# Optimization experiments

Hardware: AMD Instinct MI355X
Metric: run time of the kernel (lower is better)

Reference implementation:

```python
import jax, jax.numpy as jnp
import numpy as np

PATCH = 16
TOP_K = 5
EPS = 1e-12


def l2_normalize(x, axis):
    sq = jnp.sum(x * x, axis=axis, keepdims=True)
    return x * jax.lax.rsqrt(jnp.maximum(sq, EPS))


def patch_embed(imgs, conv_w, conv_b):
    # imgs: (P, 3, 32, 32) -> (P, n_patches=4, D=768)
    y = jax.lax.conv_general_dilated(
        imgs, conv_w, window_strides=(PATCH, PATCH), padding='VALID',
        dimension_numbers=('NCHW', 'OIHW', 'NCHW'))  # (P, D, 2, 2)
    y = y + conv_b[None, :, None, None]
    P, D = y.shape[0], y.shape[1]
    return y.reshape(P, D, -1).transpose(0, 2, 1)  # (P, 4, D)


def setup_inputs() -> dict:
    key = jax.random.key(0)
    k1, k2, k3, k4 = jax.random.split(key, 4)
    B, N, D = 256, 196, 768
    P = 32  # pool_size
    x_embed = jax.random.normal(k1, (B, N, D), dtype=jnp.float32)
    # uniform(-1, 1) init as in the torch module
    prompt = jax.random.uniform(k2, (P, 3, 32, 32), dtype=jnp.float32, minval=-1.0, maxval=1.0)
    prompt_key = jax.random.uniform(k3, (P, D), dtype=jnp.float32, minval=-1.0, maxval=1.0)
    conv_w = jax.random.normal(k4, (D, 3, PATCH, PATCH), dtype=jnp.float32) * 0.02
    conv_b = jnp.zeros((D,), dtype=jnp.float32)
    return {'x_embed': x_embed, 'prompt': prompt, 'prompt_key': prompt_key,
            'conv_w': conv_w, 'conv_b': conv_b}


def reference(x_embed, prompt, prompt_key, conv_w, conv_b):
    B = x_embed.shape[0]
    prompt_embed = patch_embed(prompt, conv_w, conv_b)      # (P, 4, D)

    x_embed_mean = jnp.mean(x_embed, axis=1)                # (B, D), embedding_key='mean'
    prompt_norm = l2_normalize(prompt_key, axis=1)          # (P, D)
    x_embed_norm = l2_normalize(x_embed_mean, axis=1)       # (B, D)
    similarity = x_embed_norm @ prompt_norm.T               # (B, P)

    _, idx = jax.lax.top_k(similarity, TOP_K)               # (B, top_k)

    batched_prompt_embed = prompt_embed[idx]                # (B, top_k, 4, D)
    Bq, K, L, D = batched_prompt_embed.shape
    batched_prompt_embed = batched_prompt_embed.reshape(Bq, K * L, D)

    batched_key_norm = prompt_norm[idx]                     # (B, top_k, D)
    reduce_sim = jnp.sum(batched_key_norm * x_embed_norm[:, None, :]) / B

    prompted_embedding = jnp.concatenate([batched_prompt_embed, x_embed], axis=1)
    return prompted_embedding, reduce_sim, similarity, idx
```

## Files before the change

kernel.cpp:

```cpp
#include <hip/hip_runtime.h>

typedef unsigned short u16;
typedef unsigned int u32;
typedef float __attribute__((ext_vector_type(4))) f32x4;

#define BB 256
#define NN 196
#define DD 768
#define PP 32
#define TOPK 5
#define NROW 216

#define OUT0_ELTS (BB * NROW * DD)
#define RS_OFF    OUT0_ELTS
#define SIM_OFF   (OUT0_ELTS + 1)
#define IDX_OFF   (OUT0_ELTS + 1 + BB * PP)

#define WS_PNORM  0
#define WS_PEMB   98304
#define WS_IDX    491520

__global__ __launch_bounds__(256) void k_prep(const float* __restrict__ pkey,
                                              const float* __restrict__ prompt,
                                              const float* __restrict__ cw,
                                              const float* __restrict__ cb,
                                              float* __restrict__ pnorm,
                                              float* __restrict__ pemb) {
    const int t = threadIdx.x;
    if (blockIdx.x < PP) {
        const int p = blockIdx.x;
        const float* row = pkey + (size_t)p * DD;
        float v0 = row[t], v1 = row[t + 256], v2 = row[t + 512];
        float sq = v0 * v0 + v1 * v1 + v2 * v2;
#pragma unroll
        for (int off = 32; off; off >>= 1) sq += __shfl_down(sq, off);
        __shared__ float wsum[4];
        __shared__ float rshared;
        if ((t & 63) == 0) wsum[t >> 6] = sq;
        __syncthreads();
        if (t == 0) rshared = rsqrtf(fmaxf(wsum[0] + wsum[1] + wsum[2] + wsum[3], 1e-12f));
        __syncthreads();
        float r = rshared;
        float* orow = pnorm + (size_t)p * DD;
        orow[t] = v0 * r;
        orow[t + 256] = v1 * r;
        orow[t + 512] = v2 * r;
    } else {
        const int bxx = blockIdx.x - PP;
        const int chunk = bxx / 32, pg = bxx - chunk * 32;
        const int m0 = pg * 4;
        const int n = chunk * 256 + t;
        __shared__ float patch[4 * DD];
        for (int idx = t; idx < 4 * DD; idx += 256) {
            const int j = idx / DD, kk = idx - j * DD;
            const int c = kk >> 8, rem = kk & 255;
            const int kh = rem >> 4, kw = rem & 15;
            const int m = m0 + j;
            const int p = m >> 2, l = m & 3;
            patch[idx] = prompt[(size_t)p * 3072 + (size_t)c * 1024
                                + ((l >> 1) * 16 + kh) * 32 + (l & 1) * 16 + kw];
        }
        __syncthreads();
        const float4* wrow = (const float4*)(cw + (size_t)n * DD);
        const float4* p0 = (const float4*)(patch);
        const float4* p1 = (const float4*)(patch + DD);
        const float4* p2 = (const float4*)(patch + 2 * DD);
        const float4* p3 = (const float4*)(patch + 3 * DD);
        float a0 = 0.f, a1 = 0.f, a2 = 0.f, a3 = 0.f;
#pragma unroll 4
        for (int kk = 0; kk < 192; ++kk) {
            const float4 w = wrow[kk];
            const float4 q0 = p0[kk], q1 = p1[kk], q2 = p2[kk], q3 = p3[kk];
            a0 += q0.x * w.x + q0.y * w.y + q0.z * w.z + q0.w * w.w;
            a1 += q1.x * w.x + q1.y * w.y + q1.z * w.z + q1.w * w.w;
            a2 += q2.x * w.x + q2.y * w.y + q2.z * w.z + q2.w * w.w;
            a3 += q3.x * w.x + q3.y * w.y + q3.z * w.z + q3.w * w.w;
        }
        const float bias = cb[n];
        pemb[(size_t)(m0 + 0) * DD + n] = a0 + bias;
        pemb[(size_t)(m0 + 1) * DD + n] = a1 + bias;
        pemb[(size_t)(m0 + 2) * DD + n] = a2 + bias;
        pemb[(size_t)(m0 + 3) * DD + n] = a3 + bias;
    }
}

__global__ __launch_bounds__(768) void k_fused(const float* __restrict__ x,
                                               const float* __restrict__ pnorm,
                                               const float* __restrict__ pemb,
                                               float* __restrict__ out,
                                               int* __restrict__ idx_ws) {
    const int b = blockIdx.x;
    const int t = threadIdx.x;
    const int g = t / 192, c = t - g * 192;
    const float* xb = x + (size_t)b * (NN * DD);
    float* ob = out + (size_t)b * (NROW * DD) + 20 * DD;
    f32x4 s = (f32x4)(0.f);
#pragma unroll
    for (int o = 0; o < 7; ++o) {
        f32x4 vv[7];
#pragma unroll
        for (int i = 0; i < 7; ++i) {
            const int row = g + 4 * (o * 7 + i);
            vv[i] = __builtin_nontemporal_load((const f32x4*)(xb + (size_t)row * DD) + c);
        }
#pragma unroll
        for (int i = 0; i < 7; ++i) {
            const int row = g + 4 * (o * 7 + i);
            s += vv[i];
            __builtin_nontemporal_store(vv[i], (f32x4*)(ob + (size_t)row * DD) + c);
        }
    }
    __shared__ f32x4 comb[768];
    __shared__ float xm[768];
    __shared__ float sims[PP];
    __shared__ float wred[12];
    __shared__ float rsh;
    __shared__ int lidx[TOPK];
    comb[g * 192 + c] = s;
    __syncthreads();
    if (g == 0) {
        f32x4 s0 = comb[c], s1 = comb[192 + c], s2 = comb[384 + c], s3 = comb[576 + c];
        const float inv = 1.0f / NN;
        f32x4 m4 = (s0 + s1 + s2 + s3) * inv;
        xm[4 * c + 0] = m4.x;
        xm[4 * c + 1] = m4.y;
        xm[4 * c + 2] = m4.z;
        xm[4 * c + 3] = m4.w;
    }
    __syncthreads();
    float sq = xm[t] * xm[t];
#pragma unroll
    for (int off = 32; off; off >>= 1) sq += __shfl_down(sq, off);
    if ((t & 63) == 0) wred[t >> 6] = sq;
    __syncthreads();
    if (t == 0) {
        float tot = 0.f;
        for (int i = 0; i < 12; ++i) tot += wred[i];
        rsh = rsqrtf(fmaxf(tot, 1e-12f));
    }
    __syncthreads();
    const float r = rsh;
    if (t < 512) {
        const int p = t >> 4, sub = t & 15;
        const float* pr = pnorm + (size_t)p * DD;
        float acc = 0.f;
#pragma unroll 8
        for (int j = 0; j < 48; ++j) {
            const int k = sub + (j << 4);
            acc += xm[k] * pr[k];
        }
        acc += __shfl_down(acc, 8, 16);
        acc += __shfl_down(acc, 4, 16);
        acc += __shfl_down(acc, 2, 16);
        acc += __shfl_down(acc, 1, 16);
        if (sub == 0) {
            const float sv = acc * r;
            sims[p] = sv;
            out[SIM_OFF + b * PP + p] = sv;
        }
    }
    __syncthreads();
    if (t < 64) {
        float v = (t < PP) ? sims[t] : -1e30f;
#pragma unroll
        for (int k = 0; k < TOPK; ++k) {
            float bv = v; int bbi = t;
#pragma unroll
            for (int off = 32; off; off >>= 1) {
                const float ov = __shfl_xor(bv, off);
                const int   oi = __shfl_xor(bbi, off);
                if (ov > bv || (ov == bv && oi < bbi)) { bv = ov; bbi = oi; }
            }
            if (t == 0) {
                lidx[k] = bbi;
                idx_ws[b * TOPK + k] = bbi;
                out[IDX_OFF + b * TOPK + k] = (float)bbi;
            }
            if (t == bbi) v = -1e30f;
        }
    }
    __syncthreads();
    f32x4* dst = (f32x4*)(out + (size_t)b * (NROW * DD));
    const f32x4* src = (const f32x4*)pemb;
    for (int v = t; v < 20 * 192; v += 768) {
        const int row = v / 192;
        const int off = v - row * 192;
        const int srow = lidx[row >> 2] * 4 + (row & 3);
        __builtin_nontemporal_store(src[srow * 192 + off], dst + row * 192 + off);
    }
}

__global__ __launch_bounds__(256) void k_final(const float* __restrict__ out_sim,
                                               const int* __restrict__ idx_ws,
                                               float* __restrict__ out_rs) {
    const int t = threadIdx.x;
    float s = 0.f;
#pragma unroll
    for (int k = 0; k < TOPK; ++k)
        s += out_sim[t * PP + idx_ws[t * TOPK + k]];
#pragma unroll
    for (int off = 32; off; off >>= 1) s += __shfl_down(s, off);
    __shared__ float wsum[4];
    if ((t & 63) == 0) wsum[t >> 6] = s;
    __syncthreads();
    if (t == 0) *out_rs = (wsum[0] + wsum[1] + wsum[2] + wsum[3]) * (1.0f / BB);
}

extern "C" void kernel_launch(void* const* d_in, const int* in_sizes, int n_in,
                              void* d_out, int out_size, void* d_ws, size_t ws_size,
                              hipStream_t stream) {
    const float* x      = (const float*)d_in[0];
    const float* prompt = (const float*)d_in[1];
    const float* pkey   = (const float*)d_in[2];
    const float* cw     = (const float*)d_in[3];
    const float* cb     = (const float*)d_in[4];
    float* out = (float*)d_out;
    char* ws = (char*)d_ws;

    float* pnorm = (float*)(ws + WS_PNORM);
    float* pemb  = (float*)(ws + WS_PEMB);
    int*   idxw  = (int*)(ws + WS_IDX);

    k_prep<<<PP + 96, 256, 0, stream>>>(pkey, prompt, cw, cb, pnorm, pemb);
    k_fused<<<BB, 768, 0, stream>>>(x, pnorm, pemb, out, idxw);
    k_final<<<1, 256, 0, stream>>>(out + SIM_OFF, idxw, out + RS_OFF);
}
```

Measured before the change: 329.8 us.

## Fuse prep, main and final kernels into one cooperative kernel with grid syncs

The three launches are merged into a single cooperative kernel. The prompt-key normalisation and the patch-embedding conv are spread across the first 64 blocks, and the conv math is interleaved with the streaming copy of x. Grid-wide syncs replace the kernel boundaries, and the reduce_sim sum now uses partials from the top-k values. This removes launch gaps and the serial prep stage, but adds two grid barriers and a cooperative-launch occupancy requirement (256 blocks of 768 threads must be co-resident).

```diff
diff --git a/kernel.cpp b/kernel.cpp
--- a/kernel.cpp
+++ b/kernel.cpp
@@ -1,7 +1,8 @@
 #include <hip/hip_runtime.h>
-
-typedef unsigned short u16;
-typedef unsigned int u32;
+#include <hip/hip_cooperative_groups.h>
+
+namespace cg = cooperative_groups;
+
 typedef float __attribute__((ext_vector_type(4))) f32x4;
 
 #define BB 256
@@ -18,110 +19,108 @@
 
 #define WS_PNORM  0
 #define WS_PEMB   98304
-#define WS_IDX    491520
-
-__global__ __launch_bounds__(256) void k_prep(const float* __restrict__ pkey,
-                                              const float* __restrict__ prompt,
-                                              const float* __restrict__ cw,
-                                              const float* __restrict__ cb,
-                                              float* __restrict__ pnorm,
-                                              float* __restrict__ pemb) {
-    const int t = threadIdx.x;
-    if (blockIdx.x < PP) {
-        const int p = blockIdx.x;
-        const float* row = pkey + (size_t)p * DD;
-        float v0 = row[t], v1 = row[t + 256], v2 = row[t + 512];
-        float sq = v0 * v0 + v1 * v1 + v2 * v2;
-#pragma unroll
-        for (int off = 32; off; off >>= 1) sq += __shfl_down(sq, off);
-        __shared__ float wsum[4];
-        __shared__ float rshared;
-        if ((t & 63) == 0) wsum[t >> 6] = sq;
-        __syncthreads();
-        if (t == 0) rshared = rsqrtf(fmaxf(wsum[0] + wsum[1] + wsum[2] + wsum[3], 1e-12f));
-        __syncthreads();
-        float r = rshared;
-        float* orow = pnorm + (size_t)p * DD;
-        orow[t] = v0 * r;
-        orow[t + 256] = v1 * r;
-        orow[t + 512] = v2 * r;
-    } else {
-        const int bxx = blockIdx.x - PP;
-        const int chunk = bxx / 32, pg = bxx - chunk * 32;
-        const int m0 = pg * 4;
-        const int n = chunk * 256 + t;
-        __shared__ float patch[4 * DD];
-        for (int idx = t; idx < 4 * DD; idx += 256) {
-            const int j = idx / DD, kk = idx - j * DD;
-            const int c = kk >> 8, rem = kk & 255;
-            const int kh = rem >> 4, kw = rem & 15;
-            const int m = m0 + j;
-            const int p = m >> 2, l = m & 3;
-            patch[idx] = prompt[(size_t)p * 3072 + (size_t)c * 1024
-                                + ((l >> 1) * 16 + kh) * 32 + (l & 1) * 16 + kw];
-        }
-        __syncthreads();
-        const float4* wrow = (const float4*)(cw + (size_t)n * DD);
-        const float4* p0 = (const float4*)(patch);
-        const float4* p1 = (const float4*)(patch + DD);
-        const float4* p2 = (const float4*)(patch + 2 * DD);
-        const float4* p3 = (const float4*)(patch + 3 * DD);
-        float a0 = 0.f, a1 = 0.f, a2 = 0.f, a3 = 0.f;
-#pragma unroll 4
-        for (int kk = 0; kk < 192; ++kk) {
-            const float4 w = wrow[kk];
-            const float4 q0 = p0[kk], q1 = p1[kk], q2 = p2[kk], q3 = p3[kk];
-            a0 += q0.x * w.x + q0.y * w.y + q0.z * w.z + q0.w * w.w;
-            a1 += q1.x * w.x + q1.y * w.y + q1.z * w.z + q1.w * w.w;
-            a2 += q2.x * w.x + q2.y * w.y + q2.z * w.z + q2.w * w.w;
-            a3 += q3.x * w.x + q3.y * w.y + q3.z * w.z + q3.w * w.w;
-        }
-        const float bias = cb[n];
-        pemb[(size_t)(m0 + 0) * DD + n] = a0 + bias;
-        pemb[(size_t)(m0 + 1) * DD + n] = a1 + bias;
-        pemb[(size_t)(m0 + 2) * DD + n] = a2 + bias;
-        pemb[(size_t)(m0 + 3) * DD + n] = a3 + bias;
-    }
-}
-
-__global__ __launch_bounds__(768) void k_fused(const float* __restrict__ x,
-                                               const float* __restrict__ pnorm,
-                                               const float* __restrict__ pemb,
-                                               float* __restrict__ out,
-                                               int* __restrict__ idx_ws) {
+#define WS_PART   491520
+
+__global__ __launch_bounds__(768, 3) void k_all(
+    const float* __restrict__ x, const float* __restrict__ prompt,
+    const float* __restrict__ pkey, const float* __restrict__ cw,
+    const float* __restrict__ cb, float* __restrict__ out,
+    float* __restrict__ pnorm, float* __restrict__ pemb,
+    float* __restrict__ wspart)
+{
     const int b = blockIdx.x;
     const int t = threadIdx.x;
-    const int g = t / 192, c = t - g * 192;
-    const float* xb = x + (size_t)b * (NN * DD);
-    float* ob = out + (size_t)b * (NROW * DD) + 20 * DD;
-    f32x4 s = (f32x4)(0.f);
-#pragma unroll
-    for (int o = 0; o < 7; ++o) {
-        f32x4 vv[7];
-#pragma unroll
-        for (int i = 0; i < 7; ++i) {
-            const int row = g + 4 * (o * 7 + i);
-            vv[i] = __builtin_nontemporal_load((const f32x4*)(xb + (size_t)row * DD) + c);
-        }
-#pragma unroll
-        for (int i = 0; i < 7; ++i) {
-            const int row = g + 4 * (o * 7 + i);
-            s += vv[i];
-            __builtin_nontemporal_store(vv[i], (f32x4*)(ob + (size_t)row * DD) + c);
-        }
-    }
+
+    __shared__ float patch[4 * DD];
     __shared__ f32x4 comb[768];
     __shared__ float xm[768];
     __shared__ float sims[PP];
     __shared__ float wred[12];
     __shared__ float rsh;
     __shared__ int lidx[TOPK];
+
+    const bool is_pemb = (b < PP);
+
+    if (b >= PP && b < 2 * PP) {
+        const int p = b - PP;
+        const float v = pkey[(size_t)p * DD + t];
+        float sq = v * v;
+#pragma unroll
+        for (int off = 32; off; off >>= 1) sq += __shfl_down(sq, off);
+        if ((t & 63) == 0) wred[t >> 6] = sq;
+        __syncthreads();
+        if (t == 0) {
+            float tot = 0.f;
+            for (int i = 0; i < 12; ++i) tot += wred[i];
+            rsh = rsqrtf(fmaxf(tot, 1e-12f));
+        }
+        __syncthreads();
+        pnorm[(size_t)p * DD + t] = v * rsh;
+    }
+
+    if (is_pemb) {
+        for (int idx = t; idx < 4 * DD; idx += 768) {
+            const int j = idx / DD, kk = idx - j * DD;
+            const int ch = kk >> 8, rem = kk & 255;
+            const int kh = rem >> 4, kw = rem & 15;
+            patch[idx] = prompt[(size_t)b * 3072 + (size_t)ch * 1024
+                                + ((j >> 1) * 16 + kh) * 32 + (j & 1) * 16 + kw];
+        }
+    }
+    __syncthreads();
+
+    const int g = t / 192, c = t - g * 192;
+    const float* xb = x + (size_t)b * (NN * DD);
+    float* ob = out + (size_t)b * (NROW * DD) + 20 * DD;
+    const float4* wrow = (const float4*)(cw + (size_t)t * DD);
+    const float4* q0p = (const float4*)(patch);
+    const float4* q1p = (const float4*)(patch + DD);
+    const float4* q2p = (const float4*)(patch + 2 * DD);
+    const float4* q3p = (const float4*)(patch + 3 * DD);
+    float a0 = 0.f, a1 = 0.f, a2 = 0.f, a3 = 0.f;
+    f32x4 s = (f32x4)(0.f);
+#pragma unroll
+    for (int o = 0; o < 7; ++o) {
+        f32x4 vv[7];
+#pragma unroll
+        for (int i = 0; i < 7; ++i) {
+            const int row = g + 4 * (o * 7 + i);
+            vv[i] = __builtin_nontemporal_load((const f32x4*)(xb + (size_t)row * DD) + c);
+        }
+        if (is_pemb) {
+            const int k0 = o * 28;
+            const int k1 = (o == 6) ? 192 : (k0 + 28);
+#pragma unroll 4
+            for (int kk = k0; kk < k1; ++kk) {
+                const float4 w = wrow[kk];
+                const float4 q0 = q0p[kk], q1 = q1p[kk], q2 = q2p[kk], q3 = q3p[kk];
+                a0 += q0.x * w.x + q0.y * w.y + q0.z * w.z + q0.w * w.w;
+                a1 += q1.x * w.x + q1.y * w.y + q1.z * w.z + q1.w * w.w;
+                a2 += q2.x * w.x + q2.y * w.y + q2.z * w.z + q2.w * w.w;
+                a3 += q3.x * w.x + q3.y * w.y + q3.z * w.z + q3.w * w.w;
+            }
+        }
+#pragma unroll
+        for (int i = 0; i < 7; ++i) {
+            const int row = g + 4 * (o * 7 + i);
+            s += vv[i];
+            __builtin_nontemporal_store(vv[i], (f32x4*)(ob + (size_t)row * DD) + c);
+        }
+    }
+    if (is_pemb) {
+        const float bias = cb[t];
+        float* pe = pemb + (size_t)(4 * b) * DD + t;
+        pe[0]      = a0 + bias;
+        pe[DD]     = a1 + bias;
+        pe[2 * DD] = a2 + bias;
+        pe[3 * DD] = a3 + bias;
+    }
+
     comb[g * 192 + c] = s;
     __syncthreads();
     if (g == 0) {
         f32x4 s0 = comb[c], s1 = comb[192 + c], s2 = comb[384 + c], s3 = comb[576 + c];
-        const float inv = 1.0f / NN;
-        f32x4 m4 = (s0 + s1 + s2 + s3) * inv;
+        f32x4 m4 = (s0 + s1 + s2 + s3) * (1.0f / NN);
         xm[4 * c + 0] = m4.x;
         xm[4 * c + 1] = m4.y;
         xm[4 * c + 2] = m4.z;
@@ -140,6 +139,10 @@
     }
     __syncthreads();
     const float r = rsh;
+
+    __threadfence();
+    cg::this_grid().sync();
+
     if (t < 512) {
         const int p = t >> 4, sub = t & 15;
         const float* pr = pnorm + (size_t)p * DD;
@@ -160,8 +163,10 @@
         }
     }
     __syncthreads();
+
     if (t < 64) {
         float v = (t < PP) ? sims[t] : -1e30f;
+        float rsum = 0.f;
 #pragma unroll
         for (int k = 0; k < TOPK; ++k) {
             float bv = v; int bbi = t;
@@ -173,13 +178,15 @@
             }
             if (t == 0) {
                 lidx[k] = bbi;
-                idx_ws[b * TOPK + k] = bbi;
                 out[IDX_OFF + b * TOPK + k] = (float)bbi;
+                rsum += bv;
             }
             if (t == bbi) v = -1e30f;
         }
-    }
-    __syncthreads();
+        if (t == 0) wspart[b] = rsum;
+    }
+    __syncthreads();
+
     f32x4* dst = (f32x4*)(out + (size_t)b * (NROW * DD));
     const f32x4* src = (const f32x4*)pemb;
     for (int v = t; v < 20 * 192; v += 768) {
@@ -188,22 +195,21 @@
         const int srow = lidx[row >> 2] * 4 + (row & 3);
         __builtin_nontemporal_store(src[srow * 192 + off], dst + row * 192 + off);
     }
-}
-
-__global__ __launch_bounds__(256) void k_final(const float* __restrict__ out_sim,
-                                               const int* __restrict__ idx_ws,
-                                               float* __restrict__ out_rs) {
-    const int t = threadIdx.x;
-    float s = 0.f;
-#pragma unroll
-    for (int k = 0; k < TOPK; ++k)
-        s += out_sim[t * PP + idx_ws[t * TOPK + k]];
-#pragma unroll
-    for (int off = 32; off; off >>= 1) s += __shfl_down(s, off);
-    __shared__ float wsum[4];
-    if ((t & 63) == 0) wsum[t >> 6] = s;
-    __syncthreads();
-    if (t == 0) *out_rs = (wsum[0] + wsum[1] + wsum[2] + wsum[3]) * (1.0f / BB);
+
+    __threadfence();
+    cg::this_grid().sync();
+    if (b == 0) {
+        float sv = (t < BB) ? wspart[t] : 0.f;
+#pragma unroll
+        for (int off = 32; off; off >>= 1) sv += __shfl_down(sv, off);
+        if ((t & 63) == 0) wred[t >> 6] = sv;
+        __syncthreads();
+        if (t == 0) {
+            float tot = 0.f;
+            for (int i = 0; i < 12; ++i) tot += wred[i];
+            out[RS_OFF] = tot * (1.0f / BB);
+        }
+    }
 }
 
 extern "C" void kernel_launch(void* const* d_in, const int* in_sizes, int n_in,
@@ -217,11 +223,11 @@
     float* out = (float*)d_out;
     char* ws = (char*)d_ws;
 
-    float* pnorm = (float*)(ws + WS_PNORM);
-    float* pemb  = (float*)(ws + WS_PEMB);
-    int*   idxw  = (int*)(ws + WS_IDX);
-
-    k_prep<<<PP + 96, 256, 0, stream>>>(pkey, prompt, cw, cb, pnorm, pemb);
-    k_fused<<<BB, 768, 0, stream>>>(x, pnorm, pemb, out, idxw);
-    k_final<<<1, 256, 0, stream>>>(out + SIM_OFF, idxw, out + RS_OFF);
+    float* pnorm  = (float*)(ws + WS_PNORM);
+    float* pemb   = (float*)(ws + WS_PEMB);
+    float* wspart = (float*)(ws + WS_PART);
+
+    void* args[] = {(void*)&x, (void*)&prompt, (void*)&pkey, (void*)&cw, (void*)&cb,
+                    (void*)&out, (void*)&pnorm, (void*)&pemb, (void*)&wspart};
+    hipLaunchCooperativeKernel((void*)k_all, dim3(BB), dim3(768), args, 0, stream);
 }
```

Result: slower. 615.9 us (+86.8%).

## Fuse key normalization and reduce_sim into main kernel, double-buffer x loads

Applied to the files above, without the earlier changes.

Drops the separate final kernel by having each block atomically add its top-k similarity sum into reduce_sim, after a memset zeroes that slot. Prompt-key normalization moves out of the prep kernel: each block recomputes the key norms alongside the similarity dot products. The x copy loop is software-pipelined so the next 7-row group is loaded while the current one is stored. This removes one launch and a workspace round trip, but adds a memset, redundant norm work in every block, and a float atomic whose summation order is nondeterministic.

```diff
diff --git a/kernel.cpp b/kernel.cpp
--- a/kernel.cpp
+++ b/kernel.cpp
@@ -1,7 +1,5 @@
 #include <hip/hip_runtime.h>
 
-typedef unsigned short u16;
-typedef unsigned int u32;
 typedef float __attribute__((ext_vector_type(4))) f32x4;
 
 #define BB 256
@@ -16,99 +14,81 @@
 #define SIM_OFF   (OUT0_ELTS + 1)
 #define IDX_OFF   (OUT0_ELTS + 1 + BB * PP)
 
-#define WS_PNORM  0
-#define WS_PEMB   98304
-#define WS_IDX    491520
+#define WS_PEMB   0
 
-__global__ __launch_bounds__(256) void k_prep(const float* __restrict__ pkey,
-                                              const float* __restrict__ prompt,
+__global__ __launch_bounds__(256) void k_prep(const float* __restrict__ prompt,
                                               const float* __restrict__ cw,
                                               const float* __restrict__ cb,
-                                              float* __restrict__ pnorm,
                                               float* __restrict__ pemb) {
     const int t = threadIdx.x;
-    if (blockIdx.x < PP) {
-        const int p = blockIdx.x;
-        const float* row = pkey + (size_t)p * DD;
-        float v0 = row[t], v1 = row[t + 256], v2 = row[t + 512];
-        float sq = v0 * v0 + v1 * v1 + v2 * v2;
-#pragma unroll
-        for (int off = 32; off; off >>= 1) sq += __shfl_down(sq, off);
-        __shared__ float wsum[4];
-        __shared__ float rshared;
-        if ((t & 63) == 0) wsum[t >> 6] = sq;
-        __syncthreads();
-        if (t == 0) rshared = rsqrtf(fmaxf(wsum[0] + wsum[1] + wsum[2] + wsum[3], 1e-12f));
-        __syncthreads();
-        float r = rshared;
-        float* orow = pnorm + (size_t)p * DD;
-        orow[t] = v0 * r;
-        orow[t + 256] = v1 * r;
-        orow[t + 512] = v2 * r;
-    } else {
-        const int bxx = blockIdx.x - PP;
-        const int chunk = bxx / 32, pg = bxx - chunk * 32;
-        const int m0 = pg * 4;
-        const int n = chunk * 256 + t;
-        __shared__ float patch[4 * DD];
-        for (int idx = t; idx < 4 * DD; idx += 256) {
-            const int j = idx / DD, kk = idx - j * DD;
-            const int c = kk >> 8, rem = kk & 255;
-            const int kh = rem >> 4, kw = rem & 15;
-            const int m = m0 + j;
-            const int p = m >> 2, l = m & 3;
-            patch[idx] = prompt[(size_t)p * 3072 + (size_t)c * 1024
-                                + ((l >> 1) * 16 + kh) * 32 + (l & 1) * 16 + kw];
-        }
-        __syncthreads();
-        const float4* wrow = (const float4*)(cw + (size_t)n * DD);
-        const float4* p0 = (const float4*)(patch);
-        const float4* p1 = (const float4*)(patch + DD);
-        const float4* p2 = (const float4*)(patch + 2 * DD);
-        const float4* p3 = (const float4*)(patch + 3 * DD);
-        float a0 = 0.f, a1 = 0.f, a2 = 0.f, a3 = 0.f;
+    const int bxx = blockIdx.x;
+    const int chunk = bxx / 32, pg = bxx - chunk * 32;
+    const int m0 = pg * 4;
+    const int n = chunk * 256 + t;
+    __shared__ float patch[4 * DD];
+    for (int idx = t; idx < 4 * DD; idx += 256) {
+        const int j = idx / DD, kk = idx - j * DD;
+        const int c = kk >> 8, rem = kk & 255;
+        const int kh = rem >> 4, kw = rem & 15;
+        const int m = m0 + j;
+        const int p = m >> 2, l = m & 3;
+        patch[idx] = prompt[(size_t)p * 3072 + (size_t)c * 1024
+                            + ((l >> 1) * 16 + kh) * 32 + (l & 1) * 16 + kw];
+    }
+    __syncthreads();
+    const float4* wrow = (const float4*)(cw + (size_t)n * DD);
+    const float4* p0 = (const float4*)(patch);
+    const float4* p1 = (const float4*)(patch + DD);
+    const float4* p2 = (const float4*)(patch + 2 * DD);
+    const float4* p3 = (const float4*)(patch + 3 * DD);
+    float a0 = 0.f, a1 = 0.f, a2 = 0.f, a3 = 0.f;
 #pragma unroll 4
-        for (int kk = 0; kk < 192; ++kk) {
-            const float4 w = wrow[kk];
-            const float4 q0 = p0[kk], q1 = p1[kk], q2 = p2[kk], q3 = p3[kk];
-            a0 += q0.x * w.x + q0.y * w.y + q0.z * w.z + q0.w * w.w;
-            a1 += q1.x * w.x + q1.y * w.y + q1.z * w.z + q1.w * w.w;
-            a2 += q2.x * w.x + q2.y * w.y + q2.z * w.z + q2.w * w.w;
-            a3 += q3.x * w.x + q3.y * w.y + q3.z * w.z + q3.w * w.w;
-        }
-        const float bias = cb[n];
-        pemb[(size_t)(m0 + 0) * DD + n] = a0 + bias;
-        pemb[(size_t)(m0 + 1) * DD + n] = a1 + bias;
-        pemb[(size_t)(m0 + 2) * DD + n] = a2 + bias;
-        pemb[(size_t)(m0 + 3) * DD + n] = a3 + bias;
+    for (int kk = 0; kk < 192; ++kk) {
+        const float4 w = wrow[kk];
+        const float4 q0 = p0[kk], q1 = p1[kk], q2 = p2[kk], q3 = p3[kk];
+        a0 += q0.x * w.x + q0.y * w.y + q0.z * w.z + q0.w * w.w;
+        a1 += q1.x * w.x + q1.y * w.y + q1.z * w.z + q1.w * w.w;
+        a2 += q2.x * w.x + q2.y * w.y + q2.z * w.z + q2.w * w.w;
+        a3 += q3.x * w.x + q3.y * w.y + q3.z * w.z + q3.w * w.w;
     }
+    const float bias = cb[n];
+    pemb[(size_t)(m0 + 0) * DD + n] = a0 + bias;
+    pemb[(size_t)(m0 + 1) * DD + n] = a1 + bias;
+    pemb[(size_t)(m0 + 2) * DD + n] = a2 + bias;
+    pemb[(size_t)(m0 + 3) * DD + n] = a3 + bias;
 }
 
 __global__ __launch_bounds__(768) void k_fused(const float* __restrict__ x,
-                                               const float* __restrict__ pnorm,
+                                               const float* __restrict__ pkey,
                                                const float* __restrict__ pemb,
-                                               float* __restrict__ out,
-                                               int* __restrict__ idx_ws) {
+                                               float* __restrict__ out) {
     const int b = blockIdx.x;
     const int t = threadIdx.x;
     const int g = t / 192, c = t - g * 192;
     const float* xb = x + (size_t)b * (NN * DD);
     float* ob = out + (size_t)b * (NROW * DD) + 20 * DD;
     f32x4 s = (f32x4)(0.f);
+    f32x4 va[7], vb[7];
+#pragma unroll
+    for (int i = 0; i < 7; ++i)
+        va[i] = __builtin_nontemporal_load((const f32x4*)(xb + (size_t)(g + 4 * i) * DD) + c);
 #pragma unroll
     for (int o = 0; o < 7; ++o) {
-        f32x4 vv[7];
+        if (o < 6) {
 #pragma unroll
-        for (int i = 0; i < 7; ++i) {
-            const int row = g + 4 * (o * 7 + i);
-            vv[i] = __builtin_nontemporal_load((const f32x4*)(xb + (size_t)row * DD) + c);
+            for (int i = 0; i < 7; ++i) {
+                const int row = g + 4 * ((o + 1) * 7 + i);
+                vb[i] = __builtin_nontemporal_load((const f32x4*)(xb + (size_t)row * DD) + c);
+            }
         }
 #pragma unroll
         for (int i = 0; i < 7; ++i) {
             const int row = g + 4 * (o * 7 + i);
-            s += vv[i];
-            __builtin_nontemporal_store(vv[i], (f32x4*)(ob + (size_t)row * DD) + c);
+            s += va[i];
+            __builtin_nontemporal_store(va[i], (f32x4*)(ob + (size_t)row * DD) + c);
         }
+#pragma unroll
+        for (int i = 0; i < 7; ++i) va[i] = vb[i];
     }
     __shared__ f32x4 comb[768];
     __shared__ float xm[768];
@@ -120,8 +100,7 @@
     __syncthreads();
     if (g == 0) {
         f32x4 s0 = comb[c], s1 = comb[192 + c], s2 = comb[384 + c], s3 = comb[576 + c];
-        const float inv = 1.0f / NN;
-        f32x4 m4 = (s0 + s1 + s2 + s3) * inv;
+        f32x4 m4 = (s0 + s1 + s2 + s3) * (1.0f / NN);
         xm[4 * c + 0] = m4.x;
         xm[4 * c + 1] = m4.y;
         xm[4 * c + 2] = m4.z;
@@ -142,19 +121,21 @@
     const float r = rsh;
     if (t < 512) {
         const int p = t >> 4, sub = t & 15;
-        const float* pr = pnorm + (size_t)p * DD;
-        float acc = 0.f;
+        const float* pr = pkey + (size_t)p * DD;
+        float acc = 0.f, nrm = 0.f;
 #pragma unroll 8
         for (int j = 0; j < 48; ++j) {
             const int k = sub + (j << 4);
-            acc += xm[k] * pr[k];
+            const float pk = pr[k];
+            acc += xm[k] * pk;
+            nrm += pk * pk;
         }
-        acc += __shfl_down(acc, 8, 16);
-        acc += __shfl_down(acc, 4, 16);
-        acc += __shfl_down(acc, 2, 16);
-        acc += __shfl_down(acc, 1, 16);
+        acc += __shfl_down(acc, 8, 16);  nrm += __shfl_down(nrm, 8, 16);
+        acc += __shfl_down(acc, 4, 16);  nrm += __shfl_down(nrm, 4, 16);
+        acc += __shfl_down(acc, 2, 16);  nrm += __shfl_down(nrm, 2, 16);
+        acc += __shfl_down(acc, 1, 16);  nrm += __shfl_down(nrm, 1, 16);
         if (sub == 0) {
-            const float sv = acc * r;
+            const float sv = acc * rsqrtf(fmaxf(nrm, 1e-12f)) * r;
             sims[p] = sv;
             out[SIM_OFF + b * PP + p] = sv;
         }
@@ -162,6 +143,7 @@
     __syncthreads();
     if (t < 64) {
         float v = (t < PP) ? sims[t] : -1e30f;
+        float rsum = 0.f;
 #pragma unroll
         for (int k = 0; k < TOPK; ++k) {
             float bv = v; int bbi = t;
@@ -173,11 +155,12 @@
             }
             if (t == 0) {
                 lidx[k] = bbi;
-                idx_ws[b * TOPK + k] = bbi;
                 out[IDX_OFF + b * TOPK + k] = (float)bbi;
+                rsum += bv;
             }
             if (t == bbi) v = -1e30f;
         }
+        if (t == 0) atomicAdd(&out[RS_OFF], rsum * (1.0f / BB));
     }
     __syncthreads();
     f32x4* dst = (f32x4*)(out + (size_t)b * (NROW * DD));
@@ -188,22 +171,6 @@
         const int srow = lidx[row >> 2] * 4 + (row & 3);
         __builtin_nontemporal_store(src[srow * 192 + off], dst + row * 192 + off);
     }
-}
-
-__global__ __launch_bounds__(256) void k_final(const float* __restrict__ out_sim,
-                                               const int* __restrict__ idx_ws,
-                                               float* __restrict__ out_rs) {
-    const int t = threadIdx.x;
-    float s = 0.f;
-#pragma unroll
-    for (int k = 0; k < TOPK; ++k)
-        s += out_sim[t * PP + idx_ws[t * TOPK + k]];
-#pragma unroll
-    for (int off = 32; off; off >>= 1) s += __shfl_down(s, off);
-    __shared__ float wsum[4];
-    if ((t & 63) == 0) wsum[t >> 6] = s;
-    __syncthreads();
-    if (t == 0) *out_rs = (wsum[0] + wsum[1] + wsum[2] + wsum[3]) * (1.0f / BB);
 }
 
 extern "C" void kernel_launch(void* const* d_in, const int* in_sizes, int n_in,
@@ -217,11 +184,9 @@
     float* out = (float*)d_out;
     char* ws = (char*)d_ws;
 
-    float* pnorm = (float*)(ws + WS_PNORM);
-    float* pemb  = (float*)(ws + WS_PEMB);
-    int*   idxw  = (int*)(ws + WS_IDX);
+    float* pemb = (float*)(ws + WS_PEMB);
 
-    k_prep<<<PP + 96, 256, 0, stream>>>(pkey, prompt, cw, cb, pnorm, pemb);
-    k_fused<<<BB, 768, 0, stream>>>(x, pnorm, pemb, out, idxw);
-    k_final<<<1, 256, 0, stream>>>(out + SIM_OFF, idxw, out + RS_OFF);
+    hipMemsetAsync(out + RS_OFF, 0, sizeof(float), stream);
+    k_prep<<<96, 256, 0, stream>>>(prompt, cw, cb, pemb);
+    k_fused<<<BB, 768, 0, stream>>>(x, pkey, pemb, out);
 }
```

After: 331.3 us. About the same (+0.4%).
